# Performance work log

Measured on AMD Instinct MI355X. Metric: run time of the kernel, lower is better.

Reference implementation:

```python
import jax, jax.numpy as jnp
import numpy as np

N, E, D = 50000, 800000, 128

def setup_inputs() -> dict:
    key = jax.random.key(0)
    ks = jax.random.split(key, 8)
    x = jax.random.normal(ks[0], (N, D), dtype=jnp.float32)
    edge_index = jax.random.randint(ks[1], (2, E), 0, N, dtype=jnp.int64)
    s2 = 1.0 / np.sqrt(2 * D)
    s4 = 1.0 / np.sqrt(4 * D)
    s1 = 1.0 / np.sqrt(D)
    pre_W = jax.random.uniform(ks[2], (2 * D, D), jnp.float32, -s2, s2)   # pre MLP (1 layer)
    pre_b = jax.random.uniform(ks[3], (D,), jnp.float32, -s2, s2)
    post_W = jax.random.uniform(ks[4], (4 * D, D), jnp.float32, -s4, s4)  # post MLP (1 layer)
    post_b = jax.random.uniform(ks[5], (D,), jnp.float32, -s4, s4)
    lin_W = jax.random.uniform(ks[6], (D, D), jnp.float32, -s1, s1)       # final projection
    lin_b = jax.random.uniform(ks[7], (D,), jnp.float32, -s1, s1)
    return {"x": x, "edge_index": edge_index, "pre_W": pre_W, "pre_b": pre_b,
            "post_W": post_W, "post_b": post_b, "lin_W": lin_W, "lin_b": lin_b}

def reference(x, edge_index, pre_W, pre_b, post_W, post_b, lin_W, lin_b):
    n = x.shape[0]
    src, dst = edge_index[0], edge_index[1]  # message flows src -> dst (source_to_target)
    # message: pre MLP on concat(x_i=target, x_j=source)  [E, 2D] -> [E, D]
    h = jnp.concatenate([x[dst], x[src]], axis=-1)
    m = h @ pre_W + pre_b
    # multi-aggregator scatter: mean, max, sum over destination nodes
    s = jax.ops.segment_sum(m, dst, num_segments=n)
    cnt = jax.ops.segment_sum(jnp.ones((m.shape[0], 1), m.dtype), dst, num_segments=n)
    mean = s / jnp.maximum(cnt, 1.0)
    mx = jax.ops.segment_max(m, dst, num_segments=n)
    mx = jnp.where(cnt > 0, mx, 0.0)  # empty segments -> 0 (PyG fill)
    aggr = jnp.concatenate([mean, mx, s], axis=-1)  # order: mean, max, sum
    # update: post MLP on concat(x, aggr)  [N, 4D] -> [N, D], then final lin
    out = jnp.concatenate([x, aggr], axis=-1) @ post_W + post_b
    out = out @ lin_W + lin_b
    # wrapper: relu + dropout (eval mode -> identity)
    return jax.nn.relu(out)
```

## Files before the change

kernel.cpp:

```cpp
#include <hip/hip_runtime.h>
#include <float.h>

#define NN 50000
#define EE 800000
#define NBKT 196
#define T1 4096
#define CAP2 8192

#define NB_CONV 3125
#define NB_PREP 385
#define NB_CNT  196
#define NB_SETUP (NB_CONV + NB_PREP + NB_CNT)

typedef __attribute__((ext_vector_type(8))) short bf16x8;
typedef __attribute__((ext_vector_type(4))) float f32x4;
typedef unsigned short u16;
typedef unsigned int u32;
typedef unsigned char u8;

__device__ __forceinline__ u16 f2bf(float f) {
  u32 u = __builtin_bit_cast(u32, f);
  u32 r = (u + 0x7fffu + ((u >> 16) & 1u)) >> 16;
  return (u16)r;
}
__device__ __forceinline__ float bflo(u32 q) { return __builtin_bit_cast(float, q << 16); }
__device__ __forceinline__ float bfhi(u32 q) { return __builtin_bit_cast(float, q & 0xffff0000u); }

__device__ __forceinline__ void gl_lds16(const u16* g, u16* l) {
  __builtin_amdgcn_global_load_lds((const __attribute__((address_space(1))) void*)g,
                                   (__attribute__((address_space(3))) void*)l, 16, 0, 0);
}

__global__ __launch_bounds__(256) void k_setup(const float* __restrict__ x,
    const float* __restrict__ post_W, const float* __restrict__ post_b,
    const float* __restrict__ lin_W, const float* __restrict__ lin_b,
    const float* __restrict__ pre_W, const int* __restrict__ ei,
    u16* __restrict__ Xcat, u16* __restrict__ WpT, u16* __restrict__ WpqT,
    float* __restrict__ bp, int* __restrict__ bucket_part) {
  __shared__ int hist[256];
  const int bid = blockIdx.x;
  const int t = threadIdx.x;
  if (bid < NB_CONV) {
    int tid = bid * 256 + t;
    int row = tid >> 4;
    int col = (tid & 15) << 3;
    const float4 v0 = *(const float4*)(x + (size_t)row * 128 + col);
    const float4 v1 = *(const float4*)(x + (size_t)row * 128 + col + 4);
    u16 tmp[8] = {f2bf(v0.x), f2bf(v0.y), f2bf(v0.z), f2bf(v0.w),
                  f2bf(v1.x), f2bf(v1.y), f2bf(v1.z), f2bf(v1.w)};
    *(bf16x8*)(Xcat + (size_t)row * 512 + col) = *(bf16x8*)tmp;
  } else if (bid < NB_CONV + NB_PREP) {
    int idx = (bid - NB_CONV) * 256 + t;
    if (idx < 512 * 128) {
      int i = idx >> 7, j = idx & 127;
      float s = 0.f;
#pragma unroll 8
      for (int c = 0; c < 128; c++) s += post_W[i * 128 + c] * lin_W[c * 128 + j];
      WpT[j * 512 + i] = f2bf(s);
    } else if (idx < 512 * 128 + 256 * 128) {
      int u = idx - 512 * 128;
      int j = u >> 7, k = u & 127;
      float v = (j < 128) ? pre_W[k * 128 + j] : pre_W[(128 + k) * 128 + (j - 128)];
      WpqT[j * 128 + k] = f2bf(v);
    } else if (idx < 512 * 128 + 256 * 128 + 128) {
      int j = idx - (512 * 128 + 256 * 128);
      float s = lin_b[j];
      for (int c = 0; c < 128; c++) s += post_b[c] * lin_W[c * 128 + j];
      bp[j] = s;
    }
  } else {
    int tile = bid - (NB_CONV + NB_PREP);
    hist[t] = 0;
    __syncthreads();
    const int e0 = tile * T1;
    const int ec = min(T1, EE - e0);
    for (int j = t; j < ec; j += 256) atomicAdd(&hist[ei[EE + e0 + j] >> 8], 1);
    __syncthreads();
    bucket_part[tile * 256 + t] = hist[t];
  }
}

__global__ void k_scanbucket(const int* __restrict__ bucket_part,
                             int* __restrict__ bucket_base,
                             int* __restrict__ bucket_cursor) {
  __shared__ int sd[256];
  int t = threadIdx.x;
  int v = 0;
#pragma unroll 4
  for (int b = 0; b < NB_CNT; ++b) v += bucket_part[b * 256 + t];
  sd[t] = v;
  __syncthreads();
  for (int s = 1; s < 256; s <<= 1) {
    int tv = (t >= s) ? sd[t - s] : 0;
    __syncthreads();
    sd[t] += tv;
    __syncthreads();
  }
  int excl = sd[t] - v;
  bucket_base[t] = excl;
  bucket_cursor[t] = excl;
}

__global__ __launch_bounds__(256) void k_bucket(const int* __restrict__ ei,
    int* __restrict__ bucket_cursor, u32* __restrict__ ebuf) {
  __shared__ u32 tilebuf[T1];
  __shared__ u32 gpos[T1];
  __shared__ int hist[256], scan_[256], runbase[256], ctr[256];
  const int t = threadIdx.x;
  const int e0 = blockIdx.x * T1;
  const int ecount = min(T1, EE - e0);
  hist[t] = 0;
  __syncthreads();
  u32 myp[16];
  int myb[16];
#pragma unroll
  for (int k = 0; k < 16; ++k) {
    int idx = t + k * 256;
    myp[k] = 0; myb[k] = 0;
    if (idx < ecount) {
      int e = e0 + idx;
      int s = ei[e], d = ei[EE + e];
      myp[k] = ((u32)d << 16) | (u32)s;
      int b = d >> 8;
      myb[k] = b;
      atomicAdd(&hist[b], 1);
    }
  }
  __syncthreads();
  int v = hist[t];
  scan_[t] = v;
  __syncthreads();
  for (int s_ = 1; s_ < 256; s_ <<= 1) {
    int tv = (t >= s_) ? scan_[t - s_] : 0;
    __syncthreads();
    scan_[t] += tv;
    __syncthreads();
  }
  int excl = scan_[t] - v;
  __syncthreads();
  scan_[t] = excl;
  ctr[t] = 0;
  if (v > 0) runbase[t] = atomicAdd(&bucket_cursor[t], v);
  __syncthreads();
#pragma unroll
  for (int k = 0; k < 16; ++k) {
    int idx = t + k * 256;
    if (idx < ecount) {
      int b = myb[k];
      int l = atomicAdd(&ctr[b], 1);
      int slot = scan_[b] + l;
      tilebuf[slot] = myp[k];
      gpos[slot] = (u32)(runbase[b] + l);
    }
  }
  __syncthreads();
  for (int j = t; j < ecount; j += 256) ebuf[gpos[j]] = tilebuf[j];
}

__global__ __launch_bounds__(256) void k_sortbucket(const u32* __restrict__ ebuf,
    const int* __restrict__ bucket_base, int* __restrict__ row_ptr,
    u16* __restrict__ csr_src) {
  __shared__ u16 sorted[CAP2];
  __shared__ int hist[256], scan_[256], ctr[256];
  const int b = blockIdx.x;
  const int t = threadIdx.x;
  const int base = bucket_base[b];
  const int end = bucket_base[b + 1];
  const int count = end - base;
  hist[t] = 0;
  __syncthreads();
  for (int j = t; j < count; j += 256) atomicAdd(&hist[(ebuf[base + j] >> 16) & 255], 1);
  __syncthreads();
  int v = hist[t];
  scan_[t] = v;
  __syncthreads();
  for (int s_ = 1; s_ < 256; s_ <<= 1) {
    int tv = (t >= s_) ? scan_[t - s_] : 0;
    __syncthreads();
    scan_[t] += tv;
    __syncthreads();
  }
  int excl = scan_[t] - v;
  __syncthreads();
  scan_[t] = excl;
  ctr[t] = 0;
  int node = b * 256 + t;
  if (node < NN) row_ptr[node] = base + excl;
  if (b == NBKT - 1 && t == 0) row_ptr[NN] = EE;
  __syncthreads();
  if (count <= CAP2) {
    for (int j = t; j < count; j += 256) {
      u32 p = ebuf[base + j];
      int ln = (p >> 16) & 255;
      int l = atomicAdd(&ctr[ln], 1);
      sorted[scan_[ln] + l] = (u16)(p & 0xffffu);
    }
    __syncthreads();
    for (int j = t; j < count; j += 256) csr_src[base + j] = sorted[j];
  } else {
    for (int j = t; j < count; j += 256) {
      u32 p = ebuf[base + j];
      int ln = (p >> 16) & 255;
      int l = atomicAdd(&ctr[ln], 1);
      csr_src[base + scan_[ln] + l] = (u16)(p & 0xffffu);
    }
  }
}

template <int KTOT, int LDA>
__device__ __forceinline__ void stage_tiles(const u16* __restrict__ A,
    const u16* __restrict__ BT, int row0, int n0, int k0,
    u16* __restrict__ As, u16* __restrict__ Bs, int t) {
#pragma unroll
  for (int it = 0; it < 4; ++it) {
    int c = t + it * 256;
    int row = c >> 3, ch = c & 7;
    gl_lds16(A + (size_t)(row0 + row) * LDA + k0 + ((ch ^ (row & 7)) << 3), As + c * 8);
  }
#pragma unroll
  for (int it = 0; it < 4; ++it) {
    int c = t + it * 256;
    int n = c >> 3, ch = c & 7;
    gl_lds16(BT + (size_t)(n0 + n) * KTOT + k0 + ((ch ^ (n & 7)) << 3), Bs + c * 8);
  }
}

__device__ __forceinline__ bf16x8 ld_frag(const u16* __restrict__ S, int rowbase,
                                          int kk, int lane) {
  int r = rowbase + (lane & 15);
  int chunk = (kk >> 3) + (lane >> 4);
  int sw = chunk ^ (r & 7);
  return *(const bf16x8*)(S + r * 64 + (sw << 3));
}

__global__ __launch_bounds__(256) void k_gemm_pq(const u16* __restrict__ Xcat,
    const u16* __restrict__ WpqT, u16* __restrict__ Pb, u8* __restrict__ Qf8) {
  __shared__ u16 As[128 * 64];
  __shared__ u16 Bs[128 * 64];
  const int t = threadIdx.x;
  const int lane = t & 63, wid = t >> 6;
  const int wr = wid >> 1, wc = wid & 1;
  const int row0 = blockIdx.x * 128;
  const int n0 = blockIdx.y * 128;
  f32x4 acc[4][4] = {};
  for (int k0 = 0; k0 < 128; k0 += 64) {
    stage_tiles<128, 512>(Xcat, WpqT, row0, n0, k0, As, Bs, t);
    __syncthreads();
#pragma unroll
    for (int kk = 0; kk < 64; kk += 32) {
      bf16x8 af[4], bg[4];
#pragma unroll
      for (int m = 0; m < 4; ++m) af[m] = ld_frag(As, wr * 64 + m * 16, kk, lane);
#pragma unroll
      for (int n = 0; n < 4; ++n) bg[n] = ld_frag(Bs, wc * 64 + n * 16, kk, lane);
#pragma unroll
      for (int m = 0; m < 4; ++m)
#pragma unroll
        for (int n = 0; n < 4; ++n)
          acc[m][n] = __builtin_amdgcn_mfma_f32_16x16x32_bf16(af[m], bg[n], acc[m][n], 0, 0, 0);
    }
    __syncthreads();
  }
  if (n0 == 0) {
#pragma unroll
    for (int m = 0; m < 4; ++m) {
      int rb = row0 + wr * 64 + m * 16 + ((lane >> 4) << 2);
#pragma unroll
      for (int n = 0; n < 4; ++n) {
        int col = wc * 64 + n * 16 + (lane & 15);
#pragma unroll
        for (int r = 0; r < 4; ++r) {
          int row = rb + r;
          if (row < NN) Pb[(size_t)row * 128 + col] = f2bf(acc[m][n][r]);
        }
      }
    }
  } else {
#pragma unroll
    for (int m = 0; m < 4; ++m) {
      int rb = row0 + wr * 64 + m * 16 + ((lane >> 4) << 2);
#pragma unroll
      for (int n = 0; n < 4; ++n) {
        int col = wc * 64 + n * 16 + (lane & 15);
#pragma unroll
        for (int r = 0; r < 4; ++r) {
          int row = rb + r;
          float v = acc[m][n][r];
          float vn = __shfl_xor(v, 1);
          u32 pk = (u32)__builtin_amdgcn_cvt_pk_fp8_f32(v, vn, 0, false);
          if (((lane & 1) == 0) && row < NN)
            *(u16*)(Qf8 + (size_t)row * 128 + col) = (u16)(pk & 0xffffu);
        }
      }
    }
  }
}

__global__ __launch_bounds__(256) void k_gemm_out(const u16* __restrict__ Xcat,
    const u16* __restrict__ WpT, const float* __restrict__ bp,
    float* __restrict__ out) {
  __shared__ u16 As[128 * 64];
  __shared__ u16 Bs[128 * 64];
  const int t = threadIdx.x;
  const int lane = t & 63, wid = t >> 6;
  const int wr = wid >> 1, wc = wid & 1;
  const int row0 = blockIdx.x * 128;
  f32x4 acc[4][4] = {};
  for (int k0 = 0; k0 < 512; k0 += 64) {
    stage_tiles<512, 512>(Xcat, WpT, row0, 0, k0, As, Bs, t);
    __syncthreads();
#pragma unroll
    for (int kk = 0; kk < 64; kk += 32) {
      bf16x8 af[4], bg[4];
#pragma unroll
      for (int m = 0; m < 4; ++m) af[m] = ld_frag(As, wr * 64 + m * 16, kk, lane);
#pragma unroll
      for (int n = 0; n < 4; ++n) bg[n] = ld_frag(Bs, wc * 64 + n * 16, kk, lane);
#pragma unroll
      for (int m = 0; m < 4; ++m)
#pragma unroll
        for (int n = 0; n < 4; ++n)
          acc[m][n] = __builtin_amdgcn_mfma_f32_16x16x32_bf16(af[m], bg[n], acc[m][n], 0, 0, 0);
    }
    __syncthreads();
  }
#pragma unroll
  for (int m = 0; m < 4; ++m) {
    int rb = row0 + wr * 64 + m * 16 + ((lane >> 4) << 2);
#pragma unroll
    for (int n = 0; n < 4; ++n) {
      int col = wc * 64 + n * 16 + (lane & 15);
      float bias = bp[col];
#pragma unroll
      for (int r = 0; r < 4; ++r) {
        int row = rb + r;
        if (row < NN) out[(size_t)row * 128 + col] = fmaxf(acc[m][n][r] + bias, 0.f);
      }
    }
  }
}

__global__ __launch_bounds__(256) void k_aggr(const u16* __restrict__ Pb,
    const u8* __restrict__ Qf8, const float* __restrict__ pre_b,
    const int* __restrict__ row_ptr, const u16* __restrict__ csr_src,
    u16* __restrict__ Xcat) {
  int wid = (blockIdx.x * 256 + threadIdx.x) >> 6;
  int lane = threadIdx.x & 63;
  if (wid >= NN) return;
  int r0 = __builtin_amdgcn_readfirstlane(row_ptr[wid]);
  int r1 = __builtin_amdgcn_readfirstlane(row_ptr[wid + 1]);
  int c = lane * 2;
  const u8* Qbase = Qf8 + c;
  float sx = 0.f, sy = 0.f, mxx = -FLT_MAX, mxy = -FLT_MAX;
  int i = r0;
  for (; i + 16 <= r1; i += 16) {
    int s[16];
#pragma unroll
    for (int k = 0; k < 16; ++k) s[k] = __builtin_amdgcn_readfirstlane((int)csr_src[i + k]);
    u32 q[16];
#pragma unroll
    for (int k = 0; k < 16; ++k) q[k] = (u32)*(const u16*)(Qbase + (size_t)s[k] * 128);
#pragma unroll
    for (int k = 0; k < 16; ++k) {
      float qx = __builtin_amdgcn_cvt_f32_fp8(q[k], 0);
      float qy = __builtin_amdgcn_cvt_f32_fp8(q[k], 1);
      sx += qx; sy += qy;
      mxx = fmaxf(mxx, qx); mxy = fmaxf(mxy, qy);
    }
  }
  if (i + 8 <= r1) {
    int s[8];
#pragma unroll
    for (int k = 0; k < 8; ++k) s[k] = __builtin_amdgcn_readfirstlane((int)csr_src[i + k]);
    u32 q[8];
#pragma unroll
    for (int k = 0; k < 8; ++k) q[k] = (u32)*(const u16*)(Qbase + (size_t)s[k] * 128);
#pragma unroll
    for (int k = 0; k < 8; ++k) {
      float qx = __builtin_amdgcn_cvt_f32_fp8(q[k], 0);
      float qy = __builtin_amdgcn_cvt_f32_fp8(q[k], 1);
      sx += qx; sy += qy;
      mxx = fmaxf(mxx, qx); mxy = fmaxf(mxy, qy);
    }
    i += 8;
  }
  if (i + 4 <= r1) {
    int s[4];
#pragma unroll
    for (int k = 0; k < 4; ++k) s[k] = __builtin_amdgcn_readfirstlane((int)csr_src[i + k]);
    u32 q[4];
#pragma unroll
    for (int k = 0; k < 4; ++k) q[k] = (u32)*(const u16*)(Qbase + (size_t)s[k] * 128);
#pragma unroll
    for (int k = 0; k < 4; ++k) {
      float qx = __builtin_amdgcn_cvt_f32_fp8(q[k], 0);
      float qy = __builtin_amdgcn_cvt_f32_fp8(q[k], 1);
      sx += qx; sy += qy;
      mxx = fmaxf(mxx, qx); mxy = fmaxf(mxy, qy);
    }
    i += 4;
  }
  for (; i < r1; ++i) {
    int s = __builtin_amdgcn_readfirstlane((int)csr_src[i]);
    u32 q = (u32)*(const u16*)(Qbase + (size_t)s * 128);
    float qx = __builtin_amdgcn_cvt_f32_fp8(q, 0);
    float qy = __builtin_amdgcn_cvt_f32_fp8(q, 1);
    sx += qx; sy += qy;
    mxx = fmaxf(mxx, qx); mxy = fmaxf(mxy, qy);
  }
  u32 pu = *(const u32*)(Pb + (size_t)wid * 128 + c);
  float2 b = *(const float2*)(pre_b + c);
  float px = bflo(pu) + b.x;
  float py = bfhi(pu) + b.y;
  int deg = r1 - r0;
  float vm_x = 0.f, vm_y = 0.f, vx_x = 0.f, vx_y = 0.f, vs_x = 0.f, vs_y = 0.f;
  if (deg > 0) {
    float inv = 1.0f / (float)deg;
    vm_x = px + sx * inv;          vm_y = py + sy * inv;
    vx_x = px + mxx;               vx_y = py + mxy;
    vs_x = (float)deg * px + sx;   vs_y = (float)deg * py + sy;
  }
  u16* arow = Xcat + (size_t)wid * 512 + 128;
  *(u32*)(arow + c)       = (u32)f2bf(vm_x) | ((u32)f2bf(vm_y) << 16);
  *(u32*)(arow + 128 + c) = (u32)f2bf(vx_x) | ((u32)f2bf(vx_y) << 16);
  *(u32*)(arow + 256 + c) = (u32)f2bf(vs_x) | ((u32)f2bf(vs_y) << 16);
}

extern "C" void kernel_launch(void* const* d_in, const int* in_sizes, int n_in,
                              void* d_out, int out_size, void* d_ws, size_t ws_size,
                              hipStream_t stream) {
  const float* x      = (const float*)d_in[0];
  const int*   ei     = (const int*)d_in[1];
  const float* pre_W  = (const float*)d_in[2];
  const float* pre_b  = (const float*)d_in[3];
  const float* post_W = (const float*)d_in[4];
  const float* post_b = (const float*)d_in[5];
  const float* lin_W  = (const float*)d_in[6];
  const float* lin_b  = (const float*)d_in[7];
  float* out = (float*)d_out;

  char* ws = (char*)d_ws;
  size_t off = 0;
  auto alloc = [&](size_t bytes) { size_t o = off; off = (off + bytes + 511) & ~(size_t)511; return o; };
  u16*   Xcat    = (u16*)(ws + alloc((size_t)NN * 512 * 2));
  u16*   Pb      = (u16*)(ws + alloc((size_t)NN * 128 * 2));
  u8*    Qf8     = (u8*)(ws + alloc((size_t)NN * 128));
  u16*   WpT     = (u16*)(ws + alloc(128 * 512 * 2));
  u16*   WpqT    = (u16*)(ws + alloc(256 * 128 * 2));
  float* bp      = (float*)(ws + alloc(128 * 4));
  int*   row_ptr = (int*)(ws + alloc((size_t)(NN + 1) * 4));
  int*   bucket_part   = (int*)(ws + alloc((size_t)NB_CNT * 256 * 4));
  int*   bucket_base   = (int*)(ws + alloc(257 * 4));
  int*   bucket_cursor = (int*)(ws + alloc(256 * 4));
  u32*   ebuf    = (u32*)(ws + alloc((size_t)EE * 4));
  u16*   csr_src = (u16*)(ws + alloc((size_t)EE * 2));
  (void)ws_size; (void)in_sizes; (void)n_in; (void)out_size;

  const int NB_M = (NN + 127) / 128;

  k_setup<<<NB_SETUP, 256, 0, stream>>>(x, post_W, post_b, lin_W, lin_b, pre_W, ei,
                                        Xcat, WpT, WpqT, bp, bucket_part);
  k_scanbucket<<<1, 256, 0, stream>>>(bucket_part, bucket_base, bucket_cursor);
  k_bucket<<<NB_CNT, 256, 0, stream>>>(ei, bucket_cursor, ebuf);
  k_sortbucket<<<NBKT, 256, 0, stream>>>(ebuf, bucket_base, row_ptr, csr_src);
  k_gemm_pq<<<dim3(NB_M, 2), 256, 0, stream>>>(Xcat, WpqT, Pb, Qf8);
  k_aggr<<<(NN * 64 + 255) / 256, 256, 0, stream>>>(Pb, Qf8, pre_b, row_ptr, csr_src, Xcat);
  k_gemm_out<<<NB_M, 256, 0, stream>>>(Xcat, WpT, bp, out);
}
```

Baseline: 124.5 us.

## Fuse scan, bucket, sort and P/Q GEMM into a persistent kernel with grid barriers

Merges the bucket scan, edge bucketing, per-bucket sort and P/Q GEMM into one persistent 512-block kernel. Phases are separated by software grid barriers built on global atomics. The scan work item runs alongside the GEMM tiles, so the GEMM work overlaps the serial single-block scan. This removes three kernel launches and their gaps, but adds spin-wait barrier overhead and relies on all 512 blocks being co-resident (launch_bounds 256,4) to avoid deadlock.

```diff
diff --git a/kernel.cpp b/kernel.cpp
--- a/kernel.cpp
+++ b/kernel.cpp
@@ -11,6 +11,8 @@
 #define NB_PREP 385
 #define NB_CNT  196
 #define NB_SETUP (NB_CONV + NB_PREP + NB_CNT)
+#define NB_GEMM 782
+#define MEGA_BLOCKS 512
 
 typedef __attribute__((ext_vector_type(8))) short bf16x8;
 typedef __attribute__((ext_vector_type(4))) float f32x4;
@@ -36,10 +38,11 @@
     const float* __restrict__ lin_W, const float* __restrict__ lin_b,
     const float* __restrict__ pre_W, const int* __restrict__ ei,
     u16* __restrict__ Xcat, u16* __restrict__ WpT, u16* __restrict__ WpqT,
-    float* __restrict__ bp, int* __restrict__ bucket_part) {
+    float* __restrict__ bp, int* __restrict__ bucket_part, int* __restrict__ bar) {
   __shared__ int hist[256];
   const int bid = blockIdx.x;
   const int t = threadIdx.x;
+  if (bid == 0 && t < 2) bar[t] = 0;
   if (bid < NB_CONV) {
     int tid = bid * 256 + t;
     int row = tid >> 4;
@@ -80,149 +83,20 @@
   }
 }
 
-__global__ void k_scanbucket(const int* __restrict__ bucket_part,
-                             int* __restrict__ bucket_base,
-                             int* __restrict__ bucket_cursor) {
-  __shared__ int sd[256];
-  int t = threadIdx.x;
-  int v = 0;
-#pragma unroll 4
-  for (int b = 0; b < NB_CNT; ++b) v += bucket_part[b * 256 + t];
-  sd[t] = v;
+__device__ __forceinline__ void gbar(int* bar, int phase) {
   __syncthreads();
-  for (int s = 1; s < 256; s <<= 1) {
-    int tv = (t >= s) ? sd[t - s] : 0;
-    __syncthreads();
-    sd[t] += tv;
-    __syncthreads();
-  }
-  int excl = sd[t] - v;
-  bucket_base[t] = excl;
-  bucket_cursor[t] = excl;
-}
-
-__global__ __launch_bounds__(256) void k_bucket(const int* __restrict__ ei,
-    int* __restrict__ bucket_cursor, u32* __restrict__ ebuf) {
-  __shared__ u32 tilebuf[T1];
-  __shared__ u32 gpos[T1];
-  __shared__ int hist[256], scan_[256], runbase[256], ctr[256];
-  const int t = threadIdx.x;
-  const int e0 = blockIdx.x * T1;
-  const int ecount = min(T1, EE - e0);
-  hist[t] = 0;
+  if (threadIdx.x == 0) {
+    __threadfence();
+    int old = __hip_atomic_fetch_add(&bar[0], 1, __ATOMIC_ACQ_REL, __HIP_MEMORY_SCOPE_AGENT);
+    if (old == phase * MEGA_BLOCKS - 1) {
+      __hip_atomic_store(&bar[1], phase, __ATOMIC_RELEASE, __HIP_MEMORY_SCOPE_AGENT);
+    } else {
+      while (__hip_atomic_load(&bar[1], __ATOMIC_ACQUIRE, __HIP_MEMORY_SCOPE_AGENT) < phase)
+        __builtin_amdgcn_s_sleep(2);
+    }
+    __threadfence();
+  }
   __syncthreads();
-  u32 myp[16];
-  int myb[16];
-#pragma unroll
-  for (int k = 0; k < 16; ++k) {
-    int idx = t + k * 256;
-    myp[k] = 0; myb[k] = 0;
-    if (idx < ecount) {
-      int e = e0 + idx;
-      int s = ei[e], d = ei[EE + e];
-      myp[k] = ((u32)d << 16) | (u32)s;
-      int b = d >> 8;
-      myb[k] = b;
-      atomicAdd(&hist[b], 1);
-    }
-  }
-  __syncthreads();
-  int v = hist[t];
-  scan_[t] = v;
-  __syncthreads();
-  for (int s_ = 1; s_ < 256; s_ <<= 1) {
-    int tv = (t >= s_) ? scan_[t - s_] : 0;
-    __syncthreads();
-    scan_[t] += tv;
-    __syncthreads();
-  }
-  int excl = scan_[t] - v;
-  __syncthreads();
-  scan_[t] = excl;
-  ctr[t] = 0;
-  if (v > 0) runbase[t] = atomicAdd(&bucket_cursor[t], v);
-  __syncthreads();
-#pragma unroll
-  for (int k = 0; k < 16; ++k) {
-    int idx = t + k * 256;
-    if (idx < ecount) {
-      int b = myb[k];
-      int l = atomicAdd(&ctr[b], 1);
-      int slot = scan_[b] + l;
-      tilebuf[slot] = myp[k];
-      gpos[slot] = (u32)(runbase[b] + l);
-    }
-  }
-  __syncthreads();
-  for (int j = t; j < ecount; j += 256) ebuf[gpos[j]] = tilebuf[j];
-}
-
-__global__ __launch_bounds__(256) void k_sortbucket(const u32* __restrict__ ebuf,
-    const int* __restrict__ bucket_base, int* __restrict__ row_ptr,
-    u16* __restrict__ csr_src) {
-  __shared__ u16 sorted[CAP2];
-  __shared__ int hist[256], scan_[256], ctr[256];
-  const int b = blockIdx.x;
-  const int t = threadIdx.x;
-  const int base = bucket_base[b];
-  const int end = bucket_base[b + 1];
-  const int count = end - base;
-  hist[t] = 0;
-  __syncthreads();
-  for (int j = t; j < count; j += 256) atomicAdd(&hist[(ebuf[base + j] >> 16) & 255], 1);
-  __syncthreads();
-  int v = hist[t];
-  scan_[t] = v;
-  __syncthreads();
-  for (int s_ = 1; s_ < 256; s_ <<= 1) {
-    int tv = (t >= s_) ? scan_[t - s_] : 0;
-    __syncthreads();
-    scan_[t] += tv;
-    __syncthreads();
-  }
-  int excl = scan_[t] - v;
-  __syncthreads();
-  scan_[t] = excl;
-  ctr[t] = 0;
-  int node = b * 256 + t;
-  if (node < NN) row_ptr[node] = base + excl;
-  if (b == NBKT - 1 && t == 0) row_ptr[NN] = EE;
-  __syncthreads();
-  if (count <= CAP2) {
-    for (int j = t; j < count; j += 256) {
-      u32 p = ebuf[base + j];
-      int ln = (p >> 16) & 255;
-      int l = atomicAdd(&ctr[ln], 1);
-      sorted[scan_[ln] + l] = (u16)(p & 0xffffu);
-    }
-    __syncthreads();
-    for (int j = t; j < count; j += 256) csr_src[base + j] = sorted[j];
-  } else {
-    for (int j = t; j < count; j += 256) {
-      u32 p = ebuf[base + j];
-      int ln = (p >> 16) & 255;
-      int l = atomicAdd(&ctr[ln], 1);
-      csr_src[base + scan_[ln] + l] = (u16)(p & 0xffffu);
-    }
-  }
-}
-
-template <int KTOT, int LDA>
-__device__ __forceinline__ void stage_tiles(const u16* __restrict__ A,
-    const u16* __restrict__ BT, int row0, int n0, int k0,
-    u16* __restrict__ As, u16* __restrict__ Bs, int t) {
-#pragma unroll
-  for (int it = 0; it < 4; ++it) {
-    int c = t + it * 256;
-    int row = c >> 3, ch = c & 7;
-    gl_lds16(A + (size_t)(row0 + row) * LDA + k0 + ((ch ^ (row & 7)) << 3), As + c * 8);
-  }
-#pragma unroll
-  for (int it = 0; it < 4; ++it) {
-    int c = t + it * 256;
-    int n = c >> 3, ch = c & 7;
-    gl_lds16(BT + (size_t)(n0 + n) * KTOT + k0 + ((ch ^ (n & 7)) << 3), Bs + c * 8);
-  }
 }
 
 __device__ __forceinline__ bf16x8 ld_frag(const u16* __restrict__ S, int rowbase,
@@ -233,64 +107,214 @@
   return *(const bf16x8*)(S + r * 64 + (sw << 3));
 }
 
-__global__ __launch_bounds__(256) void k_gemm_pq(const u16* __restrict__ Xcat,
-    const u16* __restrict__ WpqT, u16* __restrict__ Pb, u8* __restrict__ Qf8) {
-  __shared__ u16 As[128 * 64];
-  __shared__ u16 Bs[128 * 64];
+__global__ __launch_bounds__(256, 4) void k_mega(const int* __restrict__ ei,
+    const u16* __restrict__ Xcat, const u16* __restrict__ WpqT,
+    u16* __restrict__ Pb, u8* __restrict__ Qf8,
+    const int* __restrict__ bucket_part, int* __restrict__ bucket_base,
+    int* __restrict__ bucket_cursor, u32* __restrict__ ebuf,
+    int* __restrict__ row_ptr, u16* __restrict__ csr_src, int* __restrict__ bar) {
+  __shared__ __align__(16) u8 smem[36864];
   const int t = threadIdx.x;
+  const int bid = blockIdx.x;
   const int lane = t & 63, wid = t >> 6;
-  const int wr = wid >> 1, wc = wid & 1;
-  const int row0 = blockIdx.x * 128;
-  const int n0 = blockIdx.y * 128;
-  f32x4 acc[4][4] = {};
-  for (int k0 = 0; k0 < 128; k0 += 64) {
-    stage_tiles<128, 512>(Xcat, WpqT, row0, n0, k0, As, Bs, t);
-    __syncthreads();
-#pragma unroll
-    for (int kk = 0; kk < 64; kk += 32) {
-      bf16x8 af[4], bg[4];
-#pragma unroll
-      for (int m = 0; m < 4; ++m) af[m] = ld_frag(As, wr * 64 + m * 16, kk, lane);
-#pragma unroll
-      for (int n = 0; n < 4; ++n) bg[n] = ld_frag(Bs, wc * 64 + n * 16, kk, lane);
-#pragma unroll
-      for (int m = 0; m < 4; ++m)
-#pragma unroll
-        for (int n = 0; n < 4; ++n)
-          acc[m][n] = __builtin_amdgcn_mfma_f32_16x16x32_bf16(af[m], bg[n], acc[m][n], 0, 0, 0);
-    }
-    __syncthreads();
-  }
-  if (n0 == 0) {
-#pragma unroll
-    for (int m = 0; m < 4; ++m) {
-      int rb = row0 + wr * 64 + m * 16 + ((lane >> 4) << 2);
-#pragma unroll
-      for (int n = 0; n < 4; ++n) {
-        int col = wc * 64 + n * 16 + (lane & 15);
-#pragma unroll
-        for (int r = 0; r < 4; ++r) {
-          int row = rb + r;
-          if (row < NN) Pb[(size_t)row * 128 + col] = f2bf(acc[m][n][r]);
+
+  for (int u = bid; u < 1 + NB_GEMM; u += MEGA_BLOCKS) {
+    __syncthreads();
+    if (u == 0) {
+      int* sd = (int*)smem;
+      int v = 0;
+#pragma unroll 28
+      for (int b = 0; b < NB_CNT; ++b) v += bucket_part[b * 256 + t];
+      sd[t] = v;
+      __syncthreads();
+      for (int s = 1; s < 256; s <<= 1) {
+        int tv = (t >= s) ? sd[t - s] : 0;
+        __syncthreads();
+        sd[t] += tv;
+        __syncthreads();
+      }
+      int excl = sd[t] - v;
+      bucket_base[t] = excl;
+      bucket_cursor[t] = excl;
+    } else {
+      int g = u - 1;
+      int bx = g % 391, ny = g / 391;
+      u16* As = (u16*)smem;
+      u16* Bs = (u16*)(smem + 16384);
+      const int wr = wid >> 1, wc = wid & 1;
+      const int row0 = bx * 128;
+      const int n0 = ny * 128;
+      f32x4 acc[4][4] = {};
+      for (int k0 = 0; k0 < 128; k0 += 64) {
+#pragma unroll
+        for (int it = 0; it < 4; ++it) {
+          int c = t + it * 256;
+          int row = c >> 3, ch = c & 7;
+          gl_lds16(Xcat + (size_t)(row0 + row) * 512 + k0 + ((ch ^ (row & 7)) << 3), As + c * 8);
         }
-      }
-    }
-  } else {
-#pragma unroll
-    for (int m = 0; m < 4; ++m) {
-      int rb = row0 + wr * 64 + m * 16 + ((lane >> 4) << 2);
-#pragma unroll
-      for (int n = 0; n < 4; ++n) {
-        int col = wc * 64 + n * 16 + (lane & 15);
-#pragma unroll
-        for (int r = 0; r < 4; ++r) {
-          int row = rb + r;
-          float v = acc[m][n][r];
-          float vn = __shfl_xor(v, 1);
-          u32 pk = (u32)__builtin_amdgcn_cvt_pk_fp8_f32(v, vn, 0, false);
-          if (((lane & 1) == 0) && row < NN)
-            *(u16*)(Qf8 + (size_t)row * 128 + col) = (u16)(pk & 0xffffu);
+#pragma unroll
+        for (int it = 0; it < 4; ++it) {
+          int c = t + it * 256;
+          int n = c >> 3, ch = c & 7;
+          gl_lds16(WpqT + (size_t)(n0 + n) * 128 + k0 + ((ch ^ (n & 7)) << 3), Bs + c * 8);
         }
+        __syncthreads();
+#pragma unroll
+        for (int kk = 0; kk < 64; kk += 32) {
+          bf16x8 af[4], bg[4];
+#pragma unroll
+          for (int m = 0; m < 4; ++m) af[m] = ld_frag(As, wr * 64 + m * 16, kk, lane);
+#pragma unroll
+          for (int n = 0; n < 4; ++n) bg[n] = ld_frag(Bs, wc * 64 + n * 16, kk, lane);
+#pragma unroll
+          for (int m = 0; m < 4; ++m)
+#pragma unroll
+            for (int n = 0; n < 4; ++n)
+              acc[m][n] = __builtin_amdgcn_mfma_f32_16x16x32_bf16(af[m], bg[n], acc[m][n], 0, 0, 0);
+        }
+        __syncthreads();
+      }
+      if (n0 == 0) {
+#pragma unroll
+        for (int m = 0; m < 4; ++m) {
+          int rb = row0 + wr * 64 + m * 16 + ((lane >> 4) << 2);
+#pragma unroll
+          for (int n = 0; n < 4; ++n) {
+            int col = wc * 64 + n * 16 + (lane & 15);
+#pragma unroll
+            for (int r = 0; r < 4; ++r) {
+              int row = rb + r;
+              if (row < NN) Pb[(size_t)row * 128 + col] = f2bf(acc[m][n][r]);
+            }
+          }
+        }
+      } else {
+#pragma unroll
+        for (int m = 0; m < 4; ++m) {
+          int rb = row0 + wr * 64 + m * 16 + ((lane >> 4) << 2);
+#pragma unroll
+          for (int n = 0; n < 4; ++n) {
+            int col = wc * 64 + n * 16 + (lane & 15);
+#pragma unroll
+            for (int r = 0; r < 4; ++r) {
+              int row = rb + r;
+              float v = acc[m][n][r];
+              float vn = __shfl_xor(v, 1);
+              u32 pk = (u32)__builtin_amdgcn_cvt_pk_fp8_f32(v, vn, 0, false);
+              if (((lane & 1) == 0) && row < NN)
+                *(u16*)(Qf8 + (size_t)row * 128 + col) = (u16)(pk & 0xffffu);
+            }
+          }
+        }
+      }
+    }
+  }
+  gbar(bar, 1);
+
+  for (int u = bid; u < NB_CNT; u += MEGA_BLOCKS) {
+    __syncthreads();
+    u32* tilebuf = (u32*)smem;
+    u32* gpos    = (u32*)(smem + 16384);
+    int* hist    = (int*)(smem + 32768);
+    int* scn     = (int*)(smem + 33792);
+    int* runbase = (int*)(smem + 34816);
+    int* ctr     = (int*)(smem + 35840);
+    const int e0 = u * T1;
+    const int ecount = min(T1, EE - e0);
+    hist[t] = 0;
+    __syncthreads();
+    u32 myp[16];
+    int myb[16];
+#pragma unroll
+    for (int k = 0; k < 16; ++k) {
+      int idx = t + k * 256;
+      myp[k] = 0; myb[k] = 0;
+      if (idx < ecount) {
+        int e = e0 + idx;
+        int s = ei[e], d = ei[EE + e];
+        myp[k] = ((u32)d << 16) | (u32)s;
+        int b = d >> 8;
+        myb[k] = b;
+        atomicAdd(&hist[b], 1);
+      }
+    }
+    __syncthreads();
+    int v = hist[t];
+    scn[t] = v;
+    __syncthreads();
+    for (int s_ = 1; s_ < 256; s_ <<= 1) {
+      int tv = (t >= s_) ? scn[t - s_] : 0;
+      __syncthreads();
+      scn[t] += tv;
+      __syncthreads();
+    }
+    int excl = scn[t] - v;
+    __syncthreads();
+    scn[t] = excl;
+    ctr[t] = 0;
+    if (v > 0) runbase[t] = atomicAdd(&bucket_cursor[t], v);
+    __syncthreads();
+#pragma unroll
+    for (int k = 0; k < 16; ++k) {
+      int idx = t + k * 256;
+      if (idx < ecount) {
+        int b = myb[k];
+        int l = atomicAdd(&ctr[b], 1);
+        int slot = scn[b] + l;
+        tilebuf[slot] = myp[k];
+        gpos[slot] = (u32)(runbase[b] + l);
+      }
+    }
+    __syncthreads();
+    for (int j = t; j < ecount; j += 256) ebuf[gpos[j]] = tilebuf[j];
+  }
+  gbar(bar, 2);
+
+  for (int u = bid; u < NBKT; u += MEGA_BLOCKS) {
+    __syncthreads();
+    u16* sorted = (u16*)smem;
+    int* hist   = (int*)(smem + 32768);
+    int* scn    = (int*)(smem + 33792);
+    int* ctr    = (int*)(smem + 34816);
+    const int base = bucket_base[u];
+    const int end = bucket_base[u + 1];
+    const int count = end - base;
+    hist[t] = 0;
+    __syncthreads();
+    for (int j = t; j < count; j += 256) atomicAdd(&hist[(ebuf[base + j] >> 16) & 255], 1);
+    __syncthreads();
+    int v = hist[t];
+    scn[t] = v;
+    __syncthreads();
+    for (int s_ = 1; s_ < 256; s_ <<= 1) {
+      int tv = (t >= s_) ? scn[t - s_] : 0;
+      __syncthreads();
+      scn[t] += tv;
+      __syncthreads();
+    }
+    int excl = scn[t] - v;
+    __syncthreads();
+    scn[t] = excl;
+    ctr[t] = 0;
+    int node = u * 256 + t;
+    if (node < NN) row_ptr[node] = base + excl;
+    if (u == NBKT - 1 && t == 0) row_ptr[NN] = EE;
+    __syncthreads();
+    if (count <= CAP2) {
+      for (int j = t; j < count; j += 256) {
+        u32 p = ebuf[base + j];
+        int ln = (p >> 16) & 255;
+        int l = atomicAdd(&ctr[ln], 1);
+        sorted[scn[ln] + l] = (u16)(p & 0xffffu);
+      }
+      __syncthreads();
+      for (int j = t; j < count; j += 256) csr_src[base + j] = sorted[j];
+    } else {
+      for (int j = t; j < count; j += 256) {
+        u32 p = ebuf[base + j];
+        int ln = (p >> 16) & 255;
+        int l = atomicAdd(&ctr[ln], 1);
+        csr_src[base + scn[ln] + l] = (u16)(p & 0xffffu);
       }
     }
   }
@@ -307,7 +331,18 @@
   const int row0 = blockIdx.x * 128;
   f32x4 acc[4][4] = {};
   for (int k0 = 0; k0 < 512; k0 += 64) {
-    stage_tiles<512, 512>(Xcat, WpT, row0, 0, k0, As, Bs, t);
+#pragma unroll
+    for (int it = 0; it < 4; ++it) {
+      int c = t + it * 256;
+      int row = c >> 3, ch = c & 7;
+      gl_lds16(Xcat + (size_t)(row0 + row) * 512 + k0 + ((ch ^ (row & 7)) << 3), As + c * 8);
+    }
+#pragma unroll
+    for (int it = 0; it < 4; ++it) {
+      int c = t + it * 256;
+      int n = c >> 3, ch = c & 7;
+      gl_lds16(WpT + (size_t)n * 512 + k0 + ((ch ^ (n & 7)) << 3), Bs + c * 8);
+    }
     __syncthreads();
 #pragma unroll
     for (int kk = 0; kk < 64; kk += 32) {
@@ -452,6 +487,7 @@
   int*   bucket_part   = (int*)(ws + alloc((size_t)NB_CNT * 256 * 4));
   int*   bucket_base   = (int*)(ws + alloc(257 * 4));
   int*   bucket_cursor = (int*)(ws + alloc(256 * 4));
+  int*   bar     = (int*)(ws + alloc(2 * 4));
   u32*   ebuf    = (u32*)(ws + alloc((size_t)EE * 4));
   u16*   csr_src = (u16*)(ws + alloc((size_t)EE * 2));
   (void)ws_size; (void)in_sizes; (void)n_in; (void)out_size;
@@ -459,11 +495,10 @@
   const int NB_M = (NN + 127) / 128;
 
   k_setup<<<NB_SETUP, 256, 0, stream>>>(x, post_W, post_b, lin_W, lin_b, pre_W, ei,
-                                        Xcat, WpT, WpqT, bp, bucket_part);
-  k_scanbucket<<<1, 256, 0, stream>>>(bucket_part, bucket_base, bucket_cursor);
-  k_bucket<<<NB_CNT, 256, 0, stream>>>(ei, bucket_cursor, ebuf);
-  k_sortbucket<<<NBKT, 256, 0, stream>>>(ebuf, bucket_base, row_ptr, csr_src);
-  k_gemm_pq<<<dim3(NB_M, 2), 256, 0, stream>>>(Xcat, WpqT, Pb, Qf8);
+                                        Xcat, WpT, WpqT, bp, bucket_part, bar);
+  k_mega<<<MEGA_BLOCKS, 256, 0, stream>>>(ei, Xcat, WpqT, Pb, Qf8, bucket_part,
+                                          bucket_base, bucket_cursor, ebuf,
+                                          row_ptr, csr_src, bar);
   k_aggr<<<(NN * 64 + 255) / 256, 256, 0, stream>>>(Pb, Qf8, pre_b, row_ptr, csr_src, Xcat);
   k_gemm_out<<<NB_M, 256, 0, stream>>>(Xcat, WpT, bp, out);
 }
```

Result: slower. 337.2 us (+170.8%).

## Fuse x-to-bf16 conversion into the P/Q GEMM and compute both halves per block

Applied to the files above, without the earlier changes.

Removes the separate fp32-to-bf16 conversion blocks from the setup kernel. The P/Q GEMM now reads x directly, converts it to bf16, writes it both into LDS and into Xcat for the later output GEMM, and computes all 256 output columns in one 512-thread block instead of two 256-thread blocks. This saves a full read of Xcat and a second read of the activation tile, in exchange for register-staged loads in place of direct global-to-LDS loads and a larger LDS footprint per block.

```diff
diff --git a/kernel.cpp b/kernel.cpp
--- a/kernel.cpp
+++ b/kernel.cpp
@@ -7,10 +7,9 @@
 #define T1 4096
 #define CAP2 8192
 
-#define NB_CONV 3125
 #define NB_PREP 385
 #define NB_CNT  196
-#define NB_SETUP (NB_CONV + NB_PREP + NB_CNT)
+#define NB_SETUP (NB_PREP + NB_CNT)
 
 typedef __attribute__((ext_vector_type(8))) short bf16x8;
 typedef __attribute__((ext_vector_type(4))) float f32x4;
@@ -31,26 +30,16 @@
                                    (__attribute__((address_space(3))) void*)l, 16, 0, 0);
 }
 
-__global__ __launch_bounds__(256) void k_setup(const float* __restrict__ x,
-    const float* __restrict__ post_W, const float* __restrict__ post_b,
-    const float* __restrict__ lin_W, const float* __restrict__ lin_b,
-    const float* __restrict__ pre_W, const int* __restrict__ ei,
-    u16* __restrict__ Xcat, u16* __restrict__ WpT, u16* __restrict__ WpqT,
+__global__ __launch_bounds__(256) void k_setup(const float* __restrict__ post_W,
+    const float* __restrict__ post_b, const float* __restrict__ lin_W,
+    const float* __restrict__ lin_b, const float* __restrict__ pre_W,
+    const int* __restrict__ ei, u16* __restrict__ WpT, u16* __restrict__ WpqT,
     float* __restrict__ bp, int* __restrict__ bucket_part) {
   __shared__ int hist[256];
   const int bid = blockIdx.x;
   const int t = threadIdx.x;
-  if (bid < NB_CONV) {
-    int tid = bid * 256 + t;
-    int row = tid >> 4;
-    int col = (tid & 15) << 3;
-    const float4 v0 = *(const float4*)(x + (size_t)row * 128 + col);
-    const float4 v1 = *(const float4*)(x + (size_t)row * 128 + col + 4);
-    u16 tmp[8] = {f2bf(v0.x), f2bf(v0.y), f2bf(v0.z), f2bf(v0.w),
-                  f2bf(v1.x), f2bf(v1.y), f2bf(v1.z), f2bf(v1.w)};
-    *(bf16x8*)(Xcat + (size_t)row * 512 + col) = *(bf16x8*)tmp;
-  } else if (bid < NB_CONV + NB_PREP) {
-    int idx = (bid - NB_CONV) * 256 + t;
+  if (bid < NB_PREP) {
+    int idx = bid * 256 + t;
     if (idx < 512 * 128) {
       int i = idx >> 7, j = idx & 127;
       float s = 0.f;
@@ -69,7 +58,7 @@
       bp[j] = s;
     }
   } else {
-    int tile = bid - (NB_CONV + NB_PREP);
+    int tile = bid - NB_PREP;
     hist[t] = 0;
     __syncthreads();
     const int e0 = tile * T1;
@@ -207,24 +196,6 @@
   }
 }
 
-template <int KTOT, int LDA>
-__device__ __forceinline__ void stage_tiles(const u16* __restrict__ A,
-    const u16* __restrict__ BT, int row0, int n0, int k0,
-    u16* __restrict__ As, u16* __restrict__ Bs, int t) {
-#pragma unroll
-  for (int it = 0; it < 4; ++it) {
-    int c = t + it * 256;
-    int row = c >> 3, ch = c & 7;
-    gl_lds16(A + (size_t)(row0 + row) * LDA + k0 + ((ch ^ (row & 7)) << 3), As + c * 8);
-  }
-#pragma unroll
-  for (int it = 0; it < 4; ++it) {
-    int c = t + it * 256;
-    int n = c >> 3, ch = c & 7;
-    gl_lds16(BT + (size_t)(n0 + n) * KTOT + k0 + ((ch ^ (n & 7)) << 3), Bs + c * 8);
-  }
-}
-
 __device__ __forceinline__ bf16x8 ld_frag(const u16* __restrict__ S, int rowbase,
                                           int kk, int lane) {
   int r = rowbase + (lane & 15);
@@ -233,18 +204,38 @@
   return *(const bf16x8*)(S + r * 64 + (sw << 3));
 }
 
-__global__ __launch_bounds__(256) void k_gemm_pq(const u16* __restrict__ Xcat,
-    const u16* __restrict__ WpqT, u16* __restrict__ Pb, u8* __restrict__ Qf8) {
+__global__ __launch_bounds__(512) void k_gemm_pq(const float* __restrict__ x,
+    const u16* __restrict__ WpqT, u16* __restrict__ Xcat,
+    u16* __restrict__ Pb, u8* __restrict__ Qf8) {
   __shared__ u16 As[128 * 64];
-  __shared__ u16 Bs[128 * 64];
+  __shared__ u16 Bs[256 * 64];
   const int t = threadIdx.x;
   const int lane = t & 63, wid = t >> 6;
-  const int wr = wid >> 1, wc = wid & 1;
+  const int wr = wid >> 2, wc = wid & 3;
   const int row0 = blockIdx.x * 128;
-  const int n0 = blockIdx.y * 128;
   f32x4 acc[4][4] = {};
   for (int k0 = 0; k0 < 128; k0 += 64) {
-    stage_tiles<128, 512>(Xcat, WpqT, row0, n0, k0, As, Bs, t);
+#pragma unroll
+    for (int it = 0; it < 2; ++it) {
+      int c = t + it * 512;
+      int row = c >> 3, ch = c & 7;
+      int gr = row0 + row;
+      u16 tmp[8] = {};
+      if (gr < NN) {
+        const float4 v0 = *(const float4*)(x + (size_t)gr * 128 + k0 + (ch << 3));
+        const float4 v1 = *(const float4*)(x + (size_t)gr * 128 + k0 + (ch << 3) + 4);
+        tmp[0] = f2bf(v0.x); tmp[1] = f2bf(v0.y); tmp[2] = f2bf(v0.z); tmp[3] = f2bf(v0.w);
+        tmp[4] = f2bf(v1.x); tmp[5] = f2bf(v1.y); tmp[6] = f2bf(v1.z); tmp[7] = f2bf(v1.w);
+        *(bf16x8*)(Xcat + (size_t)gr * 512 + k0 + (ch << 3)) = *(bf16x8*)tmp;
+      }
+      *(bf16x8*)(As + row * 64 + ((ch ^ (row & 7)) << 3)) = *(bf16x8*)tmp;
+    }
+#pragma unroll
+    for (int it = 0; it < 4; ++it) {
+      int c = t + it * 512;
+      int n = c >> 3, ch = c & 7;
+      gl_lds16(WpqT + (size_t)n * 128 + k0 + ((ch ^ (n & 7)) << 3), Bs + c * 8);
+    }
     __syncthreads();
 #pragma unroll
     for (int kk = 0; kk < 64; kk += 32) {
@@ -261,27 +252,20 @@
     }
     __syncthreads();
   }
-  if (n0 == 0) {
-#pragma unroll
-    for (int m = 0; m < 4; ++m) {
-      int rb = row0 + wr * 64 + m * 16 + ((lane >> 4) << 2);
-#pragma unroll
-      for (int n = 0; n < 4; ++n) {
-        int col = wc * 64 + n * 16 + (lane & 15);
+#pragma unroll
+  for (int m = 0; m < 4; ++m) {
+    int rb = row0 + wr * 64 + m * 16 + ((lane >> 4) << 2);
+#pragma unroll
+    for (int n = 0; n < 4; ++n) {
+      int col = wc * 64 + n * 16 + (lane & 15);
+      if (col < 128) {
 #pragma unroll
         for (int r = 0; r < 4; ++r) {
           int row = rb + r;
           if (row < NN) Pb[(size_t)row * 128 + col] = f2bf(acc[m][n][r]);
         }
-      }
-    }
-  } else {
-#pragma unroll
-    for (int m = 0; m < 4; ++m) {
-      int rb = row0 + wr * 64 + m * 16 + ((lane >> 4) << 2);
-#pragma unroll
-      for (int n = 0; n < 4; ++n) {
-        int col = wc * 64 + n * 16 + (lane & 15);
+      } else {
+        int qc = col - 128;
 #pragma unroll
         for (int r = 0; r < 4; ++r) {
           int row = rb + r;
@@ -289,7 +273,7 @@
           float vn = __shfl_xor(v, 1);
           u32 pk = (u32)__builtin_amdgcn_cvt_pk_fp8_f32(v, vn, 0, false);
           if (((lane & 1) == 0) && row < NN)
-            *(u16*)(Qf8 + (size_t)row * 128 + col) = (u16)(pk & 0xffffu);
+            *(u16*)(Qf8 + (size_t)row * 128 + qc) = (u16)(pk & 0xffffu);
         }
       }
     }
@@ -307,7 +291,18 @@
   const int row0 = blockIdx.x * 128;
   f32x4 acc[4][4] = {};
   for (int k0 = 0; k0 < 512; k0 += 64) {
-    stage_tiles<512, 512>(Xcat, WpT, row0, 0, k0, As, Bs, t);
+#pragma unroll
+    for (int it = 0; it < 4; ++it) {
+      int c = t + it * 256;
+      int row = c >> 3, ch = c & 7;
+      gl_lds16(Xcat + (size_t)(row0 + row) * 512 + k0 + ((ch ^ (row & 7)) << 3), As + c * 8);
+    }
+#pragma unroll
+    for (int it = 0; it < 4; ++it) {
+      int c = t + it * 256;
+      int n = c >> 3, ch = c & 7;
+      gl_lds16(WpT + (size_t)n * 512 + k0 + ((ch ^ (n & 7)) << 3), Bs + c * 8);
+    }
     __syncthreads();
 #pragma unroll
     for (int kk = 0; kk < 64; kk += 32) {
@@ -458,12 +453,12 @@
 
   const int NB_M = (NN + 127) / 128;
 
-  k_setup<<<NB_SETUP, 256, 0, stream>>>(x, post_W, post_b, lin_W, lin_b, pre_W, ei,
-                                        Xcat, WpT, WpqT, bp, bucket_part);
+  k_setup<<<NB_SETUP, 256, 0, stream>>>(post_W, post_b, lin_W, lin_b, pre_W, ei,
+                                        WpT, WpqT, bp, bucket_part);
   k_scanbucket<<<1, 256, 0, stream>>>(bucket_part, bucket_base, bucket_cursor);
   k_bucket<<<NB_CNT, 256, 0, stream>>>(ei, bucket_cursor, ebuf);
   k_sortbucket<<<NBKT, 256, 0, stream>>>(ebuf, bucket_base, row_ptr, csr_src);
-  k_gemm_pq<<<dim3(NB_M, 2), 256, 0, stream>>>(Xcat, WpqT, Pb, Qf8);
+  k_gemm_pq<<<NB_M, 512, 0, stream>>>(x, WpqT, Xcat, Pb, Qf8);
   k_aggr<<<(NN * 64 + 255) / 256, 256, 0, stream>>>(Pb, Qf8, pre_b, row_ptr, csr_src, Xcat);
   k_gemm_out<<<NB_M, 256, 0, stream>>>(Xcat, WpT, bp, out);
 }
```

New measurement: 121.8 us. 2.2% less time.
